# Kernel tuning notes

Hardware: AMD Instinct MI355X
Metric: run time of the kernel (lower is better)

The kernel has to match this reference:

```python
import jax, jax.numpy as jnp
import numpy as np

P, E, N = 5, 400000, 50000  # edge types (protocols), edges per type, nodes
NEG_SLOPE = 0.2  # GATv2 leaky_relu default
LAYERS = ["e1", "e2", "e3", "d1", "d2", "d3"]  # encoder 15->8->8->2, decoder 2->8->8->15
DIMS = {"e1": (15, 8), "e2": (8, 8), "e3": (8, 2), "d1": (2, 8), "d2": (8, 8), "d3": (8, 15)}


def setup_inputs() -> dict:
    key = jax.random.key(0)
    ks = iter(jax.random.split(key, 64))

    def p(shape):
        return jax.random.normal(next(ks), shape, dtype=jnp.float32) * 0.1

    inp = {
        "x": jax.random.normal(next(ks), (N, 15), dtype=jnp.float32),
        "edge_attr": jax.random.normal(next(ks), (P, E, 35), dtype=jnp.float32),
        "edge_index": jax.random.randint(next(ks), (P, 2, E), 0, N, dtype=jnp.int32),
    }
    for name, (fi, fo) in DIMS.items():
        inp[f"{name}_wl"] = p((P, fi, fo))
        inp[f"{name}_wr"] = p((P, fi, fo))
        inp[f"{name}_we"] = p((P, 35, fo))
        inp[f"{name}_a"] = p((P, fo))
        inp[f"{name}_b"] = p((P, fo))
    return inp


def _hetero_gatv2(x, edge_index, edge_attr, Wl, Wr, We, att, b):
    """One to_hetero GATv2 layer: per-edge-type GATv2Conv (heads=1, add_self_loops=True,
    fill_value='mean' for self-loop edge_attr), summed over edge types."""
    n = x.shape[0]
    loop = jnp.arange(n, dtype=edge_index.dtype)

    def one(ei, ea, wl, wr, we, a, bb):
        xl = x @ wl  # [N, F] source-side projection
        xr = x @ wr  # [N, F] target-side projection
        s = jnp.concatenate([ei[0], loop])  # add self loops
        d = jnp.concatenate([ei[1], loop])
        # self-loop edge features = mean of edge_attr; project before concat to stay small
        eproj = jnp.concatenate(
            [ea @ we, jnp.broadcast_to(ea.mean(0) @ we, (n, wl.shape[1]))], axis=0
        )  # [E+N, F]
        m = xl[s] + xr[d] + eproj
        e = jax.nn.leaky_relu(m, NEG_SLOPE) @ a  # [E+N] attention logits
        emax = jax.ops.segment_max(e, d, num_segments=n)
        ex = jnp.exp(e - emax[d])
        den = jax.ops.segment_sum(ex, d, num_segments=n)
        alpha = ex / den[d]
        out = jax.ops.segment_sum(alpha[:, None] * xl[s], d, num_segments=n)
        return out + bb

    return jax.vmap(one)(edge_index, edge_attr, Wl, Wr, We, att, b).sum(0)


def _gae(x, edge_index, edge_attr, params):
    h = x
    for name in LAYERS:
        wl, wr, we, a, b = params[name]
        h = _hetero_gatv2(h, edge_index, edge_attr, wl, wr, we, a, b)
        if name not in ("e3", "d3"):  # relu between layers, none after enc/dec output
            h = jax.nn.relu(h)
    return h  # reconstruction [N, 15]


def reference(x, edge_attr, edge_index,
              e1_wl, e1_wr, e1_we, e1_a, e1_b,
              e2_wl, e2_wr, e2_we, e2_a, e2_b,
              e3_wl, e3_wr, e3_we, e3_a, e3_b,
              d1_wl, d1_wr, d1_we, d1_a, d1_b,
              d2_wl, d2_wr, d2_we, d2_a, d2_b,
              d3_wl, d3_wr, d3_we, d3_a, d3_b):
    params = {
        "e1": (e1_wl, e1_wr, e1_we, e1_a, e1_b),
        "e2": (e2_wl, e2_wr, e2_we, e2_a, e2_b),
        "e3": (e3_wl, e3_wr, e3_we, e3_a, e3_b),
        "d1": (d1_wl, d1_wr, d1_we, d1_a, d1_b),
        "d2": (d2_wl, d2_wr, d2_we, d2_a, d2_b),
        "d3": (d3_wl, d3_wr, d3_we, d3_a, d3_b),
    }
    return _gae(x, edge_index, edge_attr, params)
```

## Files before the change

kernel.cpp:

```cpp
#include <hip/hip_runtime.h>
#include <stdint.h>

#define PP 5
#define EE 400000
#define NN 50000
#define PN (PP*NN)
#define EPT (PP*EE)
#define G2 512
#define NGRP (EE/64)
#define NBK ((NN+255)/256)
#define NBKT (PP*NBK)
#define CHUNK 4096
#define NB2 ((EE+CHUNK-1)/CHUNK)

typedef unsigned int u32;
typedef unsigned short u16;
typedef float f32x4 __attribute__((ext_vector_type(4)));
typedef short s16x8 __attribute__((ext_vector_type(8)));
union FAB { s16x8 v; u32 w[4]; };

__device__ __forceinline__ u16 f2bf(float x){
  u32 u = __float_as_uint(x);
  u32 r = (u + 0x7fffu + ((u>>16)&1u))>>16;
  return (u16)r;
}
__device__ __forceinline__ u32 packbf(float a, float b){
  return (u32)f2bf(a) | ((u32)f2bf(b)<<16);
}
__device__ __forceinline__ float bf2f(u32 b){ return __uint_as_float(b<<16); }
__device__ __forceinline__ float lrelu(float x){ return fmaxf(x,0.f)+0.2f*fminf(x,0.f); }

__global__ __launch_bounds__(256) void k_bhist(const int* __restrict__ ei, u32* __restrict__ hist){
  __shared__ u32 sb[NBK];
  const int p=blockIdx.y, blk=blockIdx.x, t=threadIdx.x;
  for(int i=t;i<NBK;i+=256) sb[i]=0u;
  __syncthreads();
  const int* drow = ei + (size_t)(p*2+1)*EE;
  #pragma unroll
  for(int i=0;i<4;i++){
    int e = blk*CHUNK + i*1024 + t*4;
    if(e<EE){
      int4 d4=*(const int4*)&drow[e];
      atomicAdd(&sb[d4.x>>8],1u); atomicAdd(&sb[d4.y>>8],1u);
      atomicAdd(&sb[d4.z>>8],1u); atomicAdd(&sb[d4.w>>8],1u);
    }
  }
  __syncthreads();
  for(int i=t;i<NBK;i+=256) hist[((size_t)(p*NBK+i))*NB2 + blk]=sb[i];
}

__global__ __launch_bounds__(128) void k_bsum(u32* __restrict__ hist, u32* __restrict__ bcnt){
  __shared__ u32 s[128];
  const int g = blockIdx.y*NBK + blockIdx.x;
  const int t = threadIdx.x;
  u32 v = (t<NB2)? hist[(size_t)g*NB2+t] : 0u;
  s[t]=v; __syncthreads();
  for(int o=1;o<128;o<<=1){
    u32 x=(t>=o)?s[t-o]:0u;
    __syncthreads();
    s[t]+=x;
    __syncthreads();
  }
  if(t<NB2) hist[(size_t)g*NB2+t] = s[t]-v;
  if(t==127) bcnt[g]=s[127];
}

__global__ __launch_bounds__(1024) void k_bscan(const u32* __restrict__ bcnt, u32* __restrict__ boff){
  __shared__ u32 s[1024];
  const int t=threadIdx.x;
  u32 v=(t<NBKT)?bcnt[t]:0u;
  s[t]=v; __syncthreads();
  for(int o=1;o<1024;o<<=1){
    u32 x=(t>=o)?s[t-o]:0u;
    __syncthreads();
    s[t]+=x;
    __syncthreads();
  }
  if(t<NBKT) boff[t]=s[t]-v;
  if(t==0) boff[NBKT]=(u32)EPT;
}

__global__ __launch_bounds__(256) void k_bscatter2(const int* __restrict__ ei, const u32* __restrict__ boff,
                                                   const u32* __restrict__ hist, uint2* __restrict__ bedge){
  __shared__ u32 cur[NBK];
  const int p=blockIdx.y, blk=blockIdx.x, t=threadIdx.x;
  if(t<NBK) cur[t] = boff[p*NBK+t] + hist[((size_t)(p*NBK+t))*NB2 + blk];
  __syncthreads();
  const int* srow = ei + (size_t)(p*2  )*EE;
  const int* drow = ei + (size_t)(p*2+1)*EE;
  #pragma unroll
  for(int i=0;i<4;i++){
    int e = blk*CHUNK + i*1024 + t*4;
    if(e<EE){
      int4 s4=*(const int4*)&srow[e];
      int4 d4=*(const int4*)&drow[e];
      u32 p0=atomicAdd(&cur[d4.x>>8],1u);
      u32 p1=atomicAdd(&cur[d4.y>>8],1u);
      u32 p2=atomicAdd(&cur[d4.z>>8],1u);
      u32 p3=atomicAdd(&cur[d4.w>>8],1u);
      bedge[p0]=make_uint2((u32)s4.x|((u32)(d4.x&255)<<16),(u32)(e  ));
      bedge[p1]=make_uint2((u32)s4.y|((u32)(d4.y&255)<<16),(u32)(e+1));
      bedge[p2]=make_uint2((u32)s4.z|((u32)(d4.z&255)<<16),(u32)(e+2));
      bedge[p3]=make_uint2((u32)s4.w|((u32)(d4.w&255)<<16),(u32)(e+3));
    }
  }
}

__global__ __launch_bounds__(256) void k_bfinal2(const uint2* __restrict__ bedge, const u32* __restrict__ boff,
                                                 u32* __restrict__ off, uint2* __restrict__ se){
  __shared__ u32 ncnt[256];
  __shared__ u32 lcur[256];
  const int p=blockIdx.y, b=blockIdx.x, t=threadIdx.x;
  const u32 g=(u32)(p*NBK+b);
  const u32 j0=boff[g], j1=boff[g+1], cnt=j1-j0;
  ncnt[t]=0u; __syncthreads();
  for(u32 i=t;i<cnt;i+=256){
    uint2 v=bedge[j0+i];
    atomicAdd(&ncnt[(v.x>>16)&255u],1u);
  }
  __syncthreads();
  u32 myc=ncnt[t];
  for(int o=1;o<256;o<<=1){
    u32 x=(t>=o)?ncnt[t-o]:0u;
    __syncthreads();
    ncnt[t]+=x;
    __syncthreads();
  }
  const u32 excl=ncnt[t]-myc;
  const int n0=b*256;
  if(n0+t<NN) off[(size_t)p*NN + n0 + t] = j0 + excl;
  if(g==NBKT-1 && t==0) off[PN]=(u32)EPT;
  lcur[t]=j0+excl;
  __syncthreads();
  for(u32 i=t;i<cnt;i+=256){
    uint2 v=bedge[j0+i];
    u32 dl=(v.x>>16)&255u;
    u32 pos=atomicAdd(&lcur[dl],1u);
    se[pos]=make_uint2(v.x&0xffffu, v.y);
  }
}

__global__ __launch_bounds__(256) void k_split(const uint2* __restrict__ se,
                                               u32* __restrict__ srcs, u32* __restrict__ eid){
  size_t i=(size_t)blockIdx.x*256+threadIdx.x;
  if(i<EPT){ uint2 v=se[i]; srcs[i]=v.x; eid[i]=v.y; }
}

__global__ __launch_bounds__(256) void k_eproj_mfma(
    const float* __restrict__ ea, const u32* __restrict__ eid,
    const float* __restrict__ we0, const float* __restrict__ we1,
    const float* __restrict__ we2, const float* __restrict__ we3,
    const float* __restrict__ we4, const float* __restrict__ we5,
    u16* __restrict__ ep0, u16* __restrict__ ep1, u16* __restrict__ ep2,
    u16* __restrict__ ep3, u16* __restrict__ ep4, u16* __restrict__ ep5,
    float* __restrict__ bpartP)
{
  __shared__ u16  sW[64*64];
  __shared__ u16  sEpi[4*16*72];
  __shared__ float sRed[64];

  const int t=threadIdx.x, p=blockIdx.y;
  const int w=t>>6, L=t&63, e16=L&15, quad=L>>4;

  for(int i=t;i<2048;i+=256) ((u32*)sW)[i]=0u;
  if(t<64) sRed[t]=0.f;
  __syncthreads();

  #define FILLW(WPTR,FO,MOFF) { const float* wsrc=(WPTR)+(size_t)p*35*(FO); \
    for(int i=t;i<35*(FO);i+=256){ int k=i/(FO), f=i-k*(FO); \
      sW[((MOFF)+f)*64+k]=f2bf(wsrc[i]); } }
  FILLW(we0,8,0) FILLW(we1,8,8) FILLW(we2,2,16) FILLW(we3,8,24) FILLW(we4,8,32) FILLW(we5,15,48)
  #undef FILLW
  __syncthreads();

  FAB afr[4][2];
  #pragma unroll
  for(int mt=0;mt<4;mt++)
    #pragma unroll
    for(int kf=0;kf<2;kf++)
      afr[mt][kf].v = *(const s16x8*)&sW[(e16+16*mt)*64 + kf*32 + quad*8];

  float sumacc[16];
  #pragma unroll
  for(int i=0;i<16;i++) sumacc[i]=0.f;

  u16* const myEpi = &sEpi[w*1152];

  u32 eedge_next = eid[(size_t)p*EE + (size_t)blockIdx.x*64 + w*16 + e16];

  for(int g=blockIdx.x; g<NGRP; g+=G2){
    const size_t jbase = (size_t)p*EE + (size_t)g*64 + w*16;

    const u32 eedge = eedge_next;
    {
      const int gn = g + G2;
      if(gn < NGRP)
        eedge_next = eid[(size_t)p*EE + (size_t)gn*64 + w*16 + e16];
    }

    const float* row = ea + ((size_t)p*EE + eedge)*35;
    float v0=row[quad*8+0], v1=row[quad*8+1], v2=row[quad*8+2], v3=row[quad*8+3];
    float v4=row[quad*8+4], v5=row[quad*8+5], v6=row[quad*8+6], v7=row[quad*8+7];
    float b0=0.f,b1=0.f,b2=0.f;
    if(quad==0){ b0=row[32]; b1=row[33]; b2=row[34]; }

    FAB fa, fb;
    fa.w[0]=packbf(v0,v1); fa.w[1]=packbf(v2,v3);
    fa.w[2]=packbf(v4,v5); fa.w[3]=packbf(v6,v7);
    fb.w[0]=packbf(b0,b1); fb.w[1]=packbf(b2,0.f);
    fb.w[2]=0u; fb.w[3]=0u;

    f32x4 acc0={0,0,0,0},acc1={0,0,0,0},acc2={0,0,0,0},acc3={0,0,0,0};
    acc0=__builtin_amdgcn_mfma_f32_16x16x32_bf16(afr[0][0].v, fa.v, acc0,0,0,0);
    acc0=__builtin_amdgcn_mfma_f32_16x16x32_bf16(afr[0][1].v, fb.v, acc0,0,0,0);
    acc1=__builtin_amdgcn_mfma_f32_16x16x32_bf16(afr[1][0].v, fa.v, acc1,0,0,0);
    acc1=__builtin_amdgcn_mfma_f32_16x16x32_bf16(afr[1][1].v, fb.v, acc1,0,0,0);
    acc2=__builtin_amdgcn_mfma_f32_16x16x32_bf16(afr[2][0].v, fa.v, acc2,0,0,0);
    acc2=__builtin_amdgcn_mfma_f32_16x16x32_bf16(afr[2][1].v, fb.v, acc2,0,0,0);
    acc3=__builtin_amdgcn_mfma_f32_16x16x32_bf16(afr[3][0].v, fa.v, acc3,0,0,0);
    acc3=__builtin_amdgcn_mfma_f32_16x16x32_bf16(afr[3][1].v, fb.v, acc3,0,0,0);

    #pragma unroll
    for(int r=0;r<4;r++){ sumacc[r]+=acc0[r]; sumacc[4+r]+=acc1[r]; sumacc[8+r]+=acc2[r]; sumacc[12+r]+=acc3[r]; }

    {
      u16* erow=&myEpi[e16*72];
      uint2 q;
      q.x=packbf(acc0[0],acc0[1]); q.y=packbf(acc0[2],acc0[3]);
      *(uint2*)(erow +  0 + 4*quad)=q;
      q.x=packbf(acc1[0],acc1[1]); q.y=packbf(acc1[2],acc1[3]);
      *(uint2*)(erow + 16 + 4*quad)=q;
      q.x=packbf(acc2[0],acc2[1]); q.y=packbf(acc2[2],acc2[3]);
      *(uint2*)(erow + 32 + 4*quad)=q;
      q.x=packbf(acc3[0],acc3[1]); q.y=packbf(acc3[2],acc3[3]);
      *(uint2*)(erow + 48 + 4*quad)=q;
    }
    asm volatile("s_waitcnt lgkmcnt(0)" ::: "memory");

    {
      const int grp=L>>4, e=L&15;
      const u16* erow=&myEpi[e*72];
      if(grp==0)      ((uint4*)ep0)[jbase+e]=*(const uint4*)(erow+ 0);
      else if(grp==1) ((uint4*)ep1)[jbase+e]=*(const uint4*)(erow+ 8);
      else if(grp==2) ((uint4*)ep3)[jbase+e]=*(const uint4*)(erow+24);
      else            ((uint4*)ep4)[jbase+e]=*(const uint4*)(erow+32);
      if(L<32){
        const int e2=L>>1, half=L&1;
        ((uint4*)ep5)[(jbase+e2)*2+half]=*(const uint4*)(&myEpi[e2*72]+48+8*half);
      } else if(L<48){
        const int e2=L-32;
        ((u32*)ep2)[jbase+e2]=*(const u32*)(&myEpi[e2*72]+16);
      }
    }
  }

  #pragma unroll
  for(int i=0;i<16;i++){
    float v=sumacc[i];
    v+=__shfl_xor(v,1); v+=__shfl_xor(v,2); v+=__shfl_xor(v,4); v+=__shfl_xor(v,8);
    sumacc[i]=v;
  }
  if(e16==0){
    #pragma unroll
    for(int mt=0;mt<4;mt++)
      #pragma unroll
      for(int r=0;r<4;r++)
        atomicAdd(&sRed[16*mt+4*quad+r], sumacc[mt*4+r]);
  }
  __syncthreads();
  if(t<64) bpartP[((size_t)p*G2+blockIdx.x)*64+t]=sRed[t];
}

__global__ __launch_bounds__(320) void k_selfvec2(const float* __restrict__ bpartP, float* __restrict__ selfvec){
  int t=threadIdx.x;
  int p=t/64, m=t%64;
  float s=0.f;
  for(int b=0;b<G2;b++) s+=bpartP[((size_t)p*G2+b)*64+m];
  s*=(1.f/EE);
  int l=-1, f=0;
  if(m<8){l=0;f=m;} else if(m<16){l=1;f=m-8;} else if(m<18){l=2;f=m-16;}
  else if(m>=24&&m<32){l=3;f=m-24;} else if(m>=32&&m<40){l=4;f=m-32;}
  else if(m>=48&&m<63){l=5;f=m-48;}
  if(l>=0) selfvec[(size_t)(l*5+p)*16+f]=s;
}

template<int FI,int FO>
__global__ __launch_bounds__(256) void k_proj(
  const float* __restrict__ h, int hs,
  const float* __restrict__ wl, const float* __restrict__ wr,
  float* __restrict__ xl, float* __restrict__ xr)
{
  __shared__ float sl[FI*FO], sr[FI*FO];
  const int t=threadIdx.x, p=blockIdx.y;
  if(t<FI*FO){ sl[t]=wl[(size_t)p*FI*FO+t]; sr[t]=wr[(size_t)p*FI*FO+t]; }
  __syncthreads();
  const int n=blockIdx.x*256+t;
  if(n>=NN) return;
  float hv[FI];
  #pragma unroll
  for(int k=0;k<FI;k++) hv[k]=h[(size_t)n*hs+k];
  const size_t base=((size_t)p*NN+n)*FO;
  #pragma unroll
  for(int f=0;f<FO;f++){
    float al=0.f, ar=0.f;
    #pragma unroll
    for(int k=0;k<FI;k++){ al+=hv[k]*sl[k*FO+f]; ar+=hv[k]*sr[k*FO+f]; }
    xl[base+f]=al; xr[base+f]=ar;
  }
}

template<int FI,int FO,int PO,bool RELU>
__global__ __launch_bounds__(256) void k_comb(
  const float* __restrict__ partial, const float* __restrict__ b,
  const float* __restrict__ wl, const float* __restrict__ wr,
  float* __restrict__ xl, float* __restrict__ xr)
{
  __shared__ float sl[5*FI*FO], sr[5*FI*FO], sbias[FI];
  const int t=threadIdx.x;
  for(int i=t;i<5*FI*FO;i+=256){ sl[i]=wl[i]; sr[i]=wr[i]; }
  if(t<FI){ float s=0.f; for(int p=0;p<PP;p++) s+=b[p*FI+t]; sbias[t]=s; }
  __syncthreads();
  const int n=blockIdx.x*256+t;
  if(n>=NN) return;
  float h[FI];
  #pragma unroll
  for(int f=0;f<FI;f++) h[f]=sbias[f];
  #pragma unroll
  for(int p=0;p<PP;p++){
    const float* src=partial+((size_t)p*NN+n)*FI;
    #pragma unroll
    for(int f=0;f<FI;f++) h[f]+=src[f];
  }
  if(RELU){
    #pragma unroll
    for(int f=0;f<FI;f++) h[f]=fmaxf(h[f],0.f);
  }
  #pragma unroll
  for(int p=0;p<PP;p++){
    const float* wlp=&sl[p*FI*FO];
    const float* wrp=&sr[p*FI*FO];
    const size_t base=((size_t)p*NN+n)*PO;
    #pragma unroll
    for(int f=0;f<FO;f++){
      float al=0.f, ar=0.f;
      #pragma unroll
      for(int k=0;k<FI;k++){ al+=h[k]*wlp[k*FO+f]; ar+=h[k]*wrp[k*FO+f]; }
      xl[base+f]=al; xr[base+f]=ar;
    }
    #pragma unroll
    for(int f=FO;f<PO;f++){ xl[base+f]=0.f; xr[base+f]=0.f; }
  }
}

template<int FO,int PO>
__device__ __forceinline__ void load_row(const float* __restrict__ g, float* arr){
  if constexpr(FO==2){
    float2 v=*(const float2*)g; arr[0]=v.x; arr[1]=v.y;
  } else {
    #pragma unroll
    for(int c=0;c<(FO+3)/4;c++){
      float4 v=((const float4*)g)[c];
      arr[4*c]=v.x;
      if(4*c+1<FO) arr[4*c+1]=v.y;
      if(4*c+2<FO) arr[4*c+2]=v.z;
      if(4*c+3<FO) arr[4*c+3]=v.w;
    }
  }
}

template<int FO,int EPAD,int PO>
__global__ __launch_bounds__(256) void k_agg(
  const float* __restrict__ xl, const float* __restrict__ xr,
  const u32* __restrict__ off, const u32* __restrict__ srcs,
  const u16* __restrict__ ep, const float* __restrict__ avec,
  const float* __restrict__ selfv, float* __restrict__ partial)
{
  const int t=threadIdx.x, p=blockIdx.y;
  const int n=blockIdx.x*64+(t>>2), sub=t&3;
  if(n>=NN) return;
  const int r=p*NN+n;
  float av[FO], xln[FO], xrn[FO];
  #pragma unroll
  for(int f=0;f<FO;f++) av[f]=avec[p*FO+f];
  load_row<FO,PO>(xl+(size_t)r*PO, xln);
  load_row<FO,PO>(xr+(size_t)r*PO, xrn);

  float den=0.f, num[FO];
  #pragma unroll
  for(int f=0;f<FO;f++) num[f]=0.f;
  if(sub==0){
    float e=0.f;
    #pragma unroll
    for(int f=0;f<FO;f++){ float m=xln[f]+xrn[f]+selfv[p*16+f]; e+=lrelu(m)*av[f]; }
    float ex=__expf(e);
    den=ex;
    #pragma unroll
    for(int f=0;f<FO;f++) num[f]=ex*xln[f];
  }
  const u32 j1=off[r+1];
  for(u32 j=off[r]+sub;j<j1;j+=4){
    const u32 s=srcs[j];
    float epv[FO];
    if constexpr(EPAD==8){
      uint4 q=*(const uint4*)(ep+(size_t)j*8);
      epv[0]=bf2f(q.x&0xffffu); epv[1]=bf2f(q.x>>16);
      epv[2]=bf2f(q.y&0xffffu); epv[3]=bf2f(q.y>>16);
      epv[4]=bf2f(q.z&0xffffu); epv[5]=bf2f(q.z>>16);
      epv[6]=bf2f(q.w&0xffffu); epv[7]=bf2f(q.w>>16);
    } else if constexpr(EPAD==2){
      u32 q=*(const u32*)(ep+(size_t)j*2);
      epv[0]=bf2f(q&0xffffu); epv[1]=bf2f(q>>16);
    } else {
      const uint4* qq=(const uint4*)(ep+(size_t)j*16);
      uint4 q0=qq[0], q1=qq[1];
      u32 w[8]={q0.x,q0.y,q0.z,q0.w,q1.x,q1.y,q1.z,q1.w};
      #pragma unroll
      for(int i=0;i<8;i++){
        if(2*i  <FO) epv[2*i  ]=bf2f(w[i]&0xffffu);
        if(2*i+1<FO) epv[2*i+1]=bf2f(w[i]>>16);
      }
    }
    float xls[FO];
    load_row<FO,PO>(xl+((size_t)p*NN+s)*PO, xls);
    float e=0.f;
    #pragma unroll
    for(int f=0;f<FO;f++){ float m=xls[f]+xrn[f]+epv[f]; e+=lrelu(m)*av[f]; }
    const float ex=__expf(e);
    den+=ex;
    #pragma unroll
    for(int f=0;f<FO;f++) num[f]+=ex*xls[f];
  }
  den+=__shfl_xor(den,1); den+=__shfl_xor(den,2);
  #pragma unroll
  for(int f=0;f<FO;f++){ num[f]+=__shfl_xor(num[f],1); num[f]+=__shfl_xor(num[f],2); }
  if(sub==0){
    const float inv=1.f/den;
    float* dst=partial+(size_t)r*PO;
    #pragma unroll
    for(int f=0;f<FO;f++) dst[f]=num[f]*inv;
  }
}

__global__ __launch_bounds__(256) void k_final15(
  const float* __restrict__ partial, const float* __restrict__ b,
  float* __restrict__ out)
{
  __shared__ float sbias[15];
  const int t=threadIdx.x;
  if(t<15){ float s=0.f; for(int p=0;p<PP;p++) s+=b[p*15+t]; sbias[t]=s; }
  __syncthreads();
  const int n=blockIdx.x*256+t;
  if(n>=NN) return;
  float s[15];
  #pragma unroll
  for(int f=0;f<15;f++) s[f]=sbias[f];
  #pragma unroll
  for(int p=0;p<PP;p++){
    const float* src=partial+((size_t)p*NN+n)*16;
    #pragma unroll
    for(int f=0;f<15;f++) s[f]+=src[f];
  }
  #pragma unroll
  for(int f=0;f<15;f++) out[(size_t)n*15+f]=s[f];
}

extern "C" void kernel_launch(void* const* d_in, const int* in_sizes, int n_in,
                              void* d_out, int out_size, void* d_ws, size_t ws_size,
                              hipStream_t stream)
{
  const float* x =(const float*)d_in[0];
  const float* ea=(const float*)d_in[1];
  const int*   ei=(const int*)d_in[2];
  auto W=[&](int l,int k)->const float*{ return (const float*)d_in[3+5*l+k]; };

  char* base=(char*)d_ws; size_t cur=0;
  auto alloc=[&](size_t bytes)->char*{ char* pp=base+cur; cur=(cur+bytes+255)&~(size_t)255; return pp; };
  u32*  off    =(u32*) alloc((size_t)(PN+1)*4);
  u32*  hist   =(u32*) alloc((size_t)NBKT*NB2*4);
  u32*  bcnt   =(u32*) alloc((size_t)NBKT*4);
  u32*  boff   =(u32*) alloc((size_t)(NBKT+1)*4);
  u32*  srcs   =(u32*) alloc((size_t)EPT*4);
  u32*  eid    =(u32*) alloc((size_t)EPT*4);
  float* bpartP=(float*)alloc((size_t)PP*G2*64*4);
  float* selfvec=(float*)alloc(6*PP*16*4);
  float* xl    =(float*)alloc((size_t)PN*16*4);
  float* xr    =(float*)alloc((size_t)PN*16*4);
  float* partial=(float*)alloc((size_t)PN*16*4);
  u16*  ep0    =(u16*) alloc((size_t)EPT*8*2);
  u16*  ep1    =(u16*) alloc((size_t)EPT*8*2);
  u16*  ep2    =(u16*) alloc((size_t)EPT*2*2);
  u16*  ep3    =(u16*) alloc((size_t)EPT*8*2);
  u16*  ep4    =(u16*) alloc((size_t)EPT*8*2);
  u16*  ep5    =(u16*) alloc((size_t)EPT*16*2);
  uint2* bedge =(uint2*)ep5;
  uint2* se    =(uint2*)(ep5 + (size_t)EPT*8);
  (void)ws_size; (void)in_sizes; (void)n_in; (void)out_size;

  dim3 b256(256);
  k_bhist    <<<dim3(NB2,PP),b256,0,stream>>>(ei,hist);
  k_bsum     <<<dim3(NBK,PP),dim3(128),0,stream>>>(hist,bcnt);
  k_bscan    <<<dim3(1),dim3(1024),0,stream>>>(bcnt,boff);
  k_bscatter2<<<dim3(NB2,PP),b256,0,stream>>>(ei,boff,hist,bedge);
  k_bfinal2  <<<dim3(NBK,PP),b256,0,stream>>>(bedge,boff,off,se);
  k_split    <<<dim3((EPT+255)/256),b256,0,stream>>>(se,srcs,eid);
  k_eproj_mfma<<<dim3(G2,PP),b256,0,stream>>>(ea,eid,
              W(0,2),W(1,2),W(2,2),W(3,2),W(4,2),W(5,2),
              ep0,ep1,ep2,ep3,ep4,ep5,bpartP);
  k_selfvec2<<<dim3(1),dim3(320),0,stream>>>(bpartP,selfvec);

  dim3 gproj((NN+255)/256,PP), gagg((NN+63)/64,PP), gnode((NN+255)/256);

  k_proj<15,8><<<gproj,b256,0,stream>>>(x,15,W(0,0),W(0,1),xl,xr);
  k_agg<8,8,8>   <<<gagg ,b256,0,stream>>>(xl,xr,off,srcs,ep0,W(0,3),selfvec+0*80,partial);
  k_comb<8,8,8,true><<<gnode,b256,0,stream>>>(partial,W(0,4),W(1,0),W(1,1),xl,xr);
  k_agg<8,8,8>   <<<gagg ,b256,0,stream>>>(xl,xr,off,srcs,ep1,W(1,3),selfvec+1*80,partial);
  k_comb<8,2,2,true><<<gnode,b256,0,stream>>>(partial,W(1,4),W(2,0),W(2,1),xl,xr);
  k_agg<2,2,2>   <<<gagg ,b256,0,stream>>>(xl,xr,off,srcs,ep2,W(2,3),selfvec+2*80,partial);
  k_comb<2,8,8,false><<<gnode,b256,0,stream>>>(partial,W(2,4),W(3,0),W(3,1),xl,xr);
  k_agg<8,8,8>   <<<gagg ,b256,0,stream>>>(xl,xr,off,srcs,ep3,W(3,3),selfvec+3*80,partial);
  k_comb<8,8,8,true><<<gnode,b256,0,stream>>>(partial,W(3,4),W(4,0),W(4,1),xl,xr);
  k_agg<8,8,8>   <<<gagg ,b256,0,stream>>>(xl,xr,off,srcs,ep4,W(4,3),selfvec+4*80,partial);
  k_comb<8,15,16,true><<<gnode,b256,0,stream>>>(partial,W(4,4),W(5,0),W(5,1),xl,xr);
  k_agg<15,16,16><<<gagg ,b256,0,stream>>>(xl,xr,off,srcs,ep5,W(5,3),selfvec+5*80,partial);
  k_final15<<<gnode,b256,0,stream>>>(partial,W(5,4),(float*)d_out);
}
```

Baseline: 821.1 us.

## Make aggregation edge-parallel per node block with LDS atomics and compact indices

Rewrites the per-layer aggregation so each block covers 128 destination nodes. The block's threads stride over all of its CSR edges and accumulate softmax numerators and denominators with shared-memory atomics. Previously four lanes were fixed to each node, which left lanes idle on uneven degrees. Source indices are now stored as 16-bit values and a per-edge 8-bit local destination index is written directly by the bucket-finalize kernel. That removes the separate split kernel and cuts index traffic. The self-loop mean reduction is spread across 320 wavefronts, and the edge-projection grid size is changed. The cost is LDS atomic contention on high-degree nodes and reliance on node ids fitting in 16 bits.

```diff
diff --git a/kernel.cpp b/kernel.cpp
--- a/kernel.cpp
+++ b/kernel.cpp
@@ -6,15 +6,17 @@
 #define NN 50000
 #define PN (PP*NN)
 #define EPT (PP*EE)
-#define G2 512
+#define G2 408
 #define NGRP (EE/64)
 #define NBK ((NN+255)/256)
 #define NBKT (PP*NBK)
 #define CHUNK 4096
 #define NB2 ((EE+CHUNK-1)/CHUNK)
+#define NPB 128
 
 typedef unsigned int u32;
 typedef unsigned short u16;
+typedef unsigned char u8;
 typedef float f32x4 __attribute__((ext_vector_type(4)));
 typedef short s16x8 __attribute__((ext_vector_type(8)));
 union FAB { s16x8 v; u32 w[4]; };
@@ -107,7 +109,8 @@
 }
 
 __global__ __launch_bounds__(256) void k_bfinal2(const uint2* __restrict__ bedge, const u32* __restrict__ boff,
-                                                 u32* __restrict__ off, uint2* __restrict__ se){
+                                                 u32* __restrict__ off, u16* __restrict__ srcs16,
+                                                 u32* __restrict__ eid, u8* __restrict__ dst8){
   __shared__ u32 ncnt[256];
   __shared__ u32 lcur[256];
   const int p=blockIdx.y, b=blockIdx.x, t=threadIdx.x;
@@ -136,14 +139,10 @@
     uint2 v=bedge[j0+i];
     u32 dl=(v.x>>16)&255u;
     u32 pos=atomicAdd(&lcur[dl],1u);
-    se[pos]=make_uint2(v.x&0xffffu, v.y);
-  }
-}
-
-__global__ __launch_bounds__(256) void k_split(const uint2* __restrict__ se,
-                                               u32* __restrict__ srcs, u32* __restrict__ eid){
-  size_t i=(size_t)blockIdx.x*256+threadIdx.x;
-  if(i<EPT){ uint2 v=se[i]; srcs[i]=v.x; eid[i]=v.y; }
+    srcs16[pos]=(u16)(v.x&0xffffu);
+    eid[pos]=v.y;
+    dst8[pos]=(u8)dl;
+  }
 }
 
 __global__ __launch_bounds__(256) void k_eproj_mfma(
@@ -271,17 +270,21 @@
   if(t<64) bpartP[((size_t)p*G2+blockIdx.x)*64+t]=sRed[t];
 }
 
-__global__ __launch_bounds__(320) void k_selfvec2(const float* __restrict__ bpartP, float* __restrict__ selfvec){
-  int t=threadIdx.x;
-  int p=t/64, m=t%64;
+__global__ __launch_bounds__(64) void k_selfvec3(const float* __restrict__ bpartP, float* __restrict__ selfvec){
+  const int b=blockIdx.x;
+  const int p=b>>6, m=b&63, t=threadIdx.x;
   float s=0.f;
-  for(int b=0;b<G2;b++) s+=bpartP[((size_t)p*G2+b)*64+m];
-  s*=(1.f/EE);
-  int l=-1, f=0;
-  if(m<8){l=0;f=m;} else if(m<16){l=1;f=m-8;} else if(m<18){l=2;f=m-16;}
-  else if(m>=24&&m<32){l=3;f=m-24;} else if(m>=32&&m<40){l=4;f=m-32;}
-  else if(m>=48&&m<63){l=5;f=m-48;}
-  if(l>=0) selfvec[(size_t)(l*5+p)*16+f]=s;
+  for(int i=t;i<G2;i+=64) s+=bpartP[((size_t)p*G2+i)*64+m];
+  s+=__shfl_xor(s,1); s+=__shfl_xor(s,2); s+=__shfl_xor(s,4);
+  s+=__shfl_xor(s,8); s+=__shfl_xor(s,16); s+=__shfl_xor(s,32);
+  if(t==0){
+    s*=(1.f/EE);
+    int l=-1, f=0;
+    if(m<8){l=0;f=m;} else if(m<16){l=1;f=m-8;} else if(m<18){l=2;f=m-16;}
+    else if(m>=24&&m<32){l=3;f=m-24;} else if(m>=32&&m<40){l=4;f=m-32;}
+    else if(m>=48&&m<63){l=5;f=m-48;}
+    if(l>=0) selfvec[(size_t)(l*5+p)*16+f]=s;
+  }
 }
 
 template<int FI,int FO>
@@ -369,37 +372,54 @@
 }
 
 template<int FO,int EPAD,int PO>
-__global__ __launch_bounds__(256) void k_agg(
+__global__ __launch_bounds__(256) void k_agg2(
   const float* __restrict__ xl, const float* __restrict__ xr,
-  const u32* __restrict__ off, const u32* __restrict__ srcs,
-  const u16* __restrict__ ep, const float* __restrict__ avec,
-  const float* __restrict__ selfv, float* __restrict__ partial)
+  const u32* __restrict__ off, const u16* __restrict__ srcs16,
+  const u8* __restrict__ dst8, const u16* __restrict__ ep,
+  const float* __restrict__ avec, const float* __restrict__ selfv,
+  float* __restrict__ partial)
 {
+  __shared__ float sxr[NPB*FO];
+  __shared__ float sden[NPB];
+  __shared__ float snum[NPB*FO];
+  __shared__ u32   soff[NPB+1];
+
   const int t=threadIdx.x, p=blockIdx.y;
-  const int n=blockIdx.x*64+(t>>2), sub=t&3;
-  if(n>=NN) return;
-  const int r=p*NN+n;
-  float av[FO], xln[FO], xrn[FO];
+  const int n0=blockIdx.x*NPB;
+  const int nn=min(NPB, NN-n0);
+  const int qoff=n0&255;
+
+  float av[FO];
   #pragma unroll
   for(int f=0;f<FO;f++) av[f]=avec[p*FO+f];
-  load_row<FO,PO>(xl+(size_t)r*PO, xln);
-  load_row<FO,PO>(xr+(size_t)r*PO, xrn);
-
-  float den=0.f, num[FO];
-  #pragma unroll
-  for(int f=0;f<FO;f++) num[f]=0.f;
-  if(sub==0){
-    float e=0.f;
-    #pragma unroll
-    for(int f=0;f<FO;f++){ float m=xln[f]+xrn[f]+selfv[p*16+f]; e+=lrelu(m)*av[f]; }
-    float ex=__expf(e);
-    den=ex;
-    #pragma unroll
-    for(int f=0;f<FO;f++) num[f]=ex*xln[f];
-  }
-  const u32 j1=off[r+1];
-  for(u32 j=off[r]+sub;j<j1;j+=4){
-    const u32 s=srcs[j];
+
+  if(t<=nn) soff[t]=off[(size_t)p*NN+n0+t];
+  if(t<NPB){
+    if(t<nn){
+      float xrn[FO], xln[FO];
+      load_row<FO,PO>(xr+((size_t)p*NN+n0+t)*PO, xrn);
+      load_row<FO,PO>(xl+((size_t)p*NN+n0+t)*PO, xln);
+      #pragma unroll
+      for(int f=0;f<FO;f++) sxr[t*FO+f]=xrn[f];
+      float e=0.f;
+      #pragma unroll
+      for(int f=0;f<FO;f++){ float m=xln[f]+xrn[f]+selfv[p*16+f]; e+=lrelu(m)*av[f]; }
+      float ex=__expf(e);
+      sden[t]=ex;
+      #pragma unroll
+      for(int f=0;f<FO;f++) snum[t*FO+f]=ex*xln[f];
+    } else {
+      sden[t]=0.f;
+      #pragma unroll
+      for(int f=0;f<FO;f++) snum[t*FO+f]=0.f;
+    }
+  }
+  __syncthreads();
+
+  const u32 j0=soff[0], j1=soff[nn];
+  for(u32 j=j0+t; j<j1; j+=256){
+    const u32 s=srcs16[j];
+    const int dl=(int)dst8[j]-qoff;
     float epv[FO];
     if constexpr(EPAD==8){
       uint4 q=*(const uint4*)(ep+(size_t)j*8);
@@ -424,20 +444,19 @@
     load_row<FO,PO>(xl+((size_t)p*NN+s)*PO, xls);
     float e=0.f;
     #pragma unroll
-    for(int f=0;f<FO;f++){ float m=xls[f]+xrn[f]+epv[f]; e+=lrelu(m)*av[f]; }
+    for(int f=0;f<FO;f++){ float m=xls[f]+sxr[dl*FO+f]+epv[f]; e+=lrelu(m)*av[f]; }
     const float ex=__expf(e);
-    den+=ex;
-    #pragma unroll
-    for(int f=0;f<FO;f++) num[f]+=ex*xls[f];
-  }
-  den+=__shfl_xor(den,1); den+=__shfl_xor(den,2);
-  #pragma unroll
-  for(int f=0;f<FO;f++){ num[f]+=__shfl_xor(num[f],1); num[f]+=__shfl_xor(num[f],2); }
-  if(sub==0){
-    const float inv=1.f/den;
-    float* dst=partial+(size_t)r*PO;
-    #pragma unroll
-    for(int f=0;f<FO;f++) dst[f]=num[f]*inv;
+    atomicAdd(&sden[dl],ex);
+    #pragma unroll
+    for(int f=0;f<FO;f++) atomicAdd(&snum[dl*FO+f], ex*xls[f]);
+  }
+  __syncthreads();
+
+  if(t<nn){
+    const float inv=1.f/sden[t];
+    float* dst=partial+((size_t)p*NN+n0+t)*PO;
+    #pragma unroll
+    for(int f=0;f<FO;f++) dst[f]=snum[t*FO+f]*inv;
   }
 }
 
@@ -479,8 +498,9 @@
   u32*  hist   =(u32*) alloc((size_t)NBKT*NB2*4);
   u32*  bcnt   =(u32*) alloc((size_t)NBKT*4);
   u32*  boff   =(u32*) alloc((size_t)(NBKT+1)*4);
-  u32*  srcs   =(u32*) alloc((size_t)EPT*4);
+  u16*  srcs16 =(u16*) alloc((size_t)EPT*2);
   u32*  eid    =(u32*) alloc((size_t)EPT*4);
+  u8*   dst8   =(u8*)  alloc((size_t)EPT);
   float* bpartP=(float*)alloc((size_t)PP*G2*64*4);
   float* selfvec=(float*)alloc(6*PP*16*4);
   float* xl    =(float*)alloc((size_t)PN*16*4);
@@ -493,7 +513,6 @@
   u16*  ep4    =(u16*) alloc((size_t)EPT*8*2);
   u16*  ep5    =(u16*) alloc((size_t)EPT*16*2);
   uint2* bedge =(uint2*)ep5;
-  uint2* se    =(uint2*)(ep5 + (size_t)EPT*8);
   (void)ws_size; (void)in_sizes; (void)n_in; (void)out_size;
 
   dim3 b256(256);
@@ -501,26 +520,25 @@
   k_bsum     <<<dim3(NBK,PP),dim3(128),0,stream>>>(hist,bcnt);
   k_bscan    <<<dim3(1),dim3(1024),0,stream>>>(bcnt,boff);
   k_bscatter2<<<dim3(NB2,PP),b256,0,stream>>>(ei,boff,hist,bedge);
-  k_bfinal2  <<<dim3(NBK,PP),b256,0,stream>>>(bedge,boff,off,se);
-  k_split    <<<dim3((EPT+255)/256),b256,0,stream>>>(se,srcs,eid);
+  k_bfinal2  <<<dim3(NBK,PP),b256,0,stream>>>(bedge,boff,off,srcs16,eid,dst8);
   k_eproj_mfma<<<dim3(G2,PP),b256,0,stream>>>(ea,eid,
               W(0,2),W(1,2),W(2,2),W(3,2),W(4,2),W(5,2),
               ep0,ep1,ep2,ep3,ep4,ep5,bpartP);
-  k_selfvec2<<<dim3(1),dim3(320),0,stream>>>(bpartP,selfvec);
-
-  dim3 gproj((NN+255)/256,PP), gagg((NN+63)/64,PP), gnode((NN+255)/256);
+  k_selfvec3<<<dim3(PP*64),dim3(64),0,stream>>>(bpartP,selfvec);
+
+  dim3 gproj((NN+255)/256,PP), gagg((NN+NPB-1)/NPB,PP), gnode((NN+255)/256);
 
   k_proj<15,8><<<gproj,b256,0,stream>>>(x,15,W(0,0),W(0,1),xl,xr);
-  k_agg<8,8,8>   <<<gagg ,b256,0,stream>>>(xl,xr,off,srcs,ep0,W(0,3),selfvec+0*80,partial);
+  k_agg2<8,8,8>   <<<gagg ,b256,0,stream>>>(xl,xr,off,srcs16,dst8,ep0,W(0,3),selfvec+0*80,partial);
   k_comb<8,8,8,true><<<gnode,b256,0,stream>>>(partial,W(0,4),W(1,0),W(1,1),xl,xr);
-  k_agg<8,8,8>   <<<gagg ,b256,0,stream>>>(xl,xr,off,srcs,ep1,W(1,3),selfvec+1*80,partial);
+  k_agg2<8,8,8>   <<<gagg ,b256,0,stream>>>(xl,xr,off,srcs16,dst8,ep1,W(1,3),selfvec+1*80,partial);
   k_comb<8,2,2,true><<<gnode,b256,0,stream>>>(partial,W(1,4),W(2,0),W(2,1),xl,xr);
-  k_agg<2,2,2>   <<<gagg ,b256,0,stream>>>(xl,xr,off,srcs,ep2,W(2,3),selfvec+2*80,partial);
+  k_agg2<2,2,2>   <<<gagg ,b256,0,stream>>>(xl,xr,off,srcs16,dst8,ep2,W(2,3),selfvec+2*80,partial);
   k_comb<2,8,8,false><<<gnode,b256,0,stream>>>(partial,W(2,4),W(3,0),W(3,1),xl,xr);
-  k_agg<8,8,8>   <<<gagg ,b256,0,stream>>>(xl,xr,off,srcs,ep3,W(3,3),selfvec+3*80,partial);
+  k_agg2<8,8,8>   <<<gagg ,b256,0,stream>>>(xl,xr,off,srcs16,dst8,ep3,W(3,3),selfvec+3*80,partial);
   k_comb<8,8,8,true><<<gnode,b256,0,stream>>>(partial,W(3,4),W(4,0),W(4,1),xl,xr);
-  k_agg<8,8,8>   <<<gagg ,b256,0,stream>>>(xl,xr,off,srcs,ep4,W(4,3),selfvec+4*80,partial);
+  k_agg2<8,8,8>   <<<gagg ,b256,0,stream>>>(xl,xr,off,srcs16,dst8,ep4,W(4,3),selfvec+4*80,partial);
   k_comb<8,15,16,true><<<gnode,b256,0,stream>>>(partial,W(4,4),W(5,0),W(5,1),xl,xr);
-  k_agg<15,16,16><<<gagg ,b256,0,stream>>>(xl,xr,off,srcs,ep5,W(5,3),selfvec+5*80,partial);
+  k_agg2<15,16,16><<<gagg ,b256,0,stream>>>(xl,xr,off,srcs16,dst8,ep5,W(5,3),selfvec+5*80,partial);
   k_final15<<<gnode,b256,0,stream>>>(partial,W(5,4),(float*)d_out);
 }
```

Result: slower. 1.417 ms (+72.6%).
